# Performance work log

Measured on AMD Instinct MI355X. Metric: run time of the kernel, lower is better.

The kernel has to match this reference:

```python
import jax, jax.numpy as jnp
import numpy as np

B, P = 8, 768
S = 36                 # sample_points (also deformable offset pairs)
C_IN, C_ADJ = 64, 72   # prior_feat_channels -> adjusted channels
D, G = 512, 4          # fc_hidden_dim, num_groups (= attention heads)
N_OFFSETS, N_STRIPS, DEG = 72, 71, 3


def _bilinear(img, x, y):
    """img: [B,H,W,C]; x,y: [B,N] pixel coords. Bilinear sample, zeros outside."""
    H, W = img.shape[1], img.shape[2]
    x0 = jnp.floor(x); y0 = jnp.floor(y)
    x0i = x0.astype(jnp.int32); y0i = y0.astype(jnp.int32)
    wx1 = x - x0; wy1 = y - y0

    def corner(xi, yi, w):
        valid = (xi >= 0) & (xi < W) & (yi >= 0) & (yi < H)
        xc = jnp.clip(xi, 0, W - 1); yc = jnp.clip(yi, 0, H - 1)
        vals = jax.vmap(lambda f, yy, xx: f[yy, xx])(img, yc, xc)  # [B,N,C]
        return vals * (w * valid)[..., None]

    return (corner(x0i, y0i, (1 - wx1) * (1 - wy1))
            + corner(x0i + 1, y0i, wx1 * (1 - wy1))
            + corner(x0i, y0i + 1, (1 - wx1) * wy1)
            + corner(x0i + 1, y0i + 1, wx1 * wy1))


def _resize_ac(img, Ht, Wt):
    """Bilinear resize with align_corners=True. img: [B,H,W,C]."""
    Bsz, H, W, _ = img.shape
    gy, gx = jnp.meshgrid(jnp.linspace(0.0, H - 1.0, Ht),
                          jnp.linspace(0.0, W - 1.0, Wt), indexing='ij')
    xf = jnp.broadcast_to(gx.reshape(-1), (Bsz, Ht * Wt))
    yf = jnp.broadcast_to(gy.reshape(-1), (Bsz, Ht * Wt))
    return _bilinear(img, xf, yf).reshape(Bsz, Ht, Wt, -1)


def setup_inputs():
    ks = jax.random.split(jax.random.key(0), 32)
    r = lambda i, shp, s=1.0: jax.random.normal(ks[i], shp, dtype=jnp.float32) * s
    z = lambda shp: jnp.zeros(shp, jnp.float32)
    return {
        'feat0': r(0, (B, C_IN, 40, 100)),
        'feat1': r(1, (B, C_IN, 20, 50)),
        'feat2': r(2, (B, C_IN, 10, 25)),
        'priors': jax.random.uniform(ks[3], (B, P, 4 + N_OFFSETS), dtype=jnp.float32) * N_STRIPS,
        'ca_w': r(4, (C_ADJ, C_IN), 0.125), 'ca_b': z((C_ADJ,)),
        'off_w': r(5, (2 * S, C_ADJ), 0.01), 'off_b': r(6, (2 * S,), 0.01),
        'dp_w': r(7, (C_ADJ, C_ADJ), 0.167), 'dp_b': z((C_ADJ,)),
        'z_emb': r(8, (S,), 0.3) + 1.0,
        'gf_w': r(9, (D, S // G, C_ADJ), 0.02), 'gf_b': z((D,)),
        'wq': r(10, (D, D), 0.044), 'bq': z((D,)),
        'wk': r(11, (D, D), 0.044), 'bk': z((D,)),
        'wv': r(12, (D, D), 0.044), 'bv': z((D,)),
        'wo': r(13, (D, D), 0.044), 'bo': z((D,)),
        'cf_w1': r(14, (2 * D, D), 0.044), 'cf_b1': z((2 * D,)),
        'cf_w2': r(15, (D, 2 * D), 0.031), 'cf_b2': z((D,)),
        'cls_w1': r(16, (D, D), 0.044), 'cls_b1': z((D,)),
        'cls_w2': r(17, (2, D), 0.001), 'cls_b2': z((2,)),
        'reg_w1': r(18, (D, D), 0.044), 'reg_b1': z((D,)),
        'p_w1': r(19, (2 * D, D), 0.044), 'p_b1': z((2 * D,)),
        'p_w2': r(20, (DEG + 1, 2 * D), 0.031), 'p_b2': z((DEG + 1,)),
        'b_scale': jnp.ones((1,), jnp.float32), 'b_bias': z((1,)),
    }


def reference(feat0, feat1, feat2, priors, ca_w, ca_b, off_w, off_b, dp_w, dp_b,
              z_emb, gf_w, gf_b, wq, bq, wk, bk, wv, bv, wo, bo,
              cf_w1, cf_b1, cf_w2, cf_b2, cls_w1, cls_b1, cls_w2, cls_b2,
              reg_w1, reg_b1, p_w1, p_b1, p_w2, p_b2, b_scale, b_bias):
    f32 = jnp.float32
    lin = lambda x, w, b: x @ w.T + b

    # ---- prior sampling grid (CLRNet-style) ----
    sx_idx = jnp.floor(jnp.linspace(0.0, 1.0, S) * N_STRIPS).astype(jnp.int32)
    pf_ys = jnp.flip(1.0 - sx_idx.astype(f32) / N_STRIPS)            # [S]
    pf_xs = priors[..., 4 + sx_idx][:, :, ::-1]                       # [B,P,S]
    gx = jnp.clip(pf_xs / N_STRIPS, 0.0, 1.0) * 2.0 - 1.0            # [-1,1]
    gy = jnp.broadcast_to(pf_ys * 2.0 - 1.0, gx.shape)

    # ---- channel adjust (1x1 conv) per level, channels-last ----
    adj = lambda f: jnp.einsum('bchw,oc->bhwo', f, ca_w) + ca_b
    feats = [adj(feat0), adj(feat1), adj(feat2)]                      # [B,H,W,C_ADJ]
    offs0 = jnp.einsum('bhwc,oc->bhwo', feats[0], off_w) + off_b     # [B,H0,W0,2S]

    # ---- deformable multi-level sampling: per (prior, point) gather + 1x1 proj ----
    sidx = jnp.arange(S)
    levels = []
    for l, fl in enumerate(feats):
        Hl, Wl = fl.shape[1], fl.shape[2]
        offs = offs0 if l == 0 else _resize_ac(offs0, Hl, Wl)
        px = (gx + 1.0) * 0.5 * (Wl - 1)
        py = (gy + 1.0) * 0.5 * (Hl - 1)
        ov = _bilinear(offs, px.reshape(B, -1), py.reshape(B, -1)).reshape(B, P, S, S, 2)
        dyx = ov[:, :, sidx, sidx, :]                                 # offset pair s for point s
        sxp = (px + dyx[..., 1]).reshape(B, -1)
        syp = (py + dyx[..., 0]).reshape(B, -1)
        smp = _bilinear(fl, sxp, syp).reshape(B, P, S, C_ADJ)
        levels.append(smp @ dp_w.T + dp_b)
    feat_all = jnp.stack(levels)                                      # [3,B,P,S,C]

    # ---- z-embedding soft level selection ----
    zw = jax.nn.softmax(-(z_emb[:, None] - jnp.arange(3, dtype=f32)) ** 2 / 2.0, axis=-1)  # [S,3]
    feature = jnp.einsum('lbpsc,sl->bpsc', feat_all, zw)

    # ---- grouped gather Conv1d(S -> D, kernel=C_ADJ, groups=G) ----
    xg = feature.reshape(B * P, G, S // G, C_ADJ)
    wg = gf_w.reshape(G, D // G, S // G, C_ADJ)
    feature = (jnp.einsum('ngik,goik->ngo', xg, wg).reshape(B * P, D) + gf_b).reshape(B, P, D)

    # ---- multi-head self-attention over priors + channel MLP residual ----
    dh = D // G
    q = lin(feature, wq, bq).reshape(B, P, G, dh).transpose(0, 2, 1, 3)
    k = lin(feature, wk, bk).reshape(B, P, G, dh).transpose(0, 2, 1, 3)
    v = lin(feature, wv, bv).reshape(B, P, G, dh).transpose(0, 2, 1, 3)
    attn = jax.nn.softmax(jnp.einsum('bgqd,bgkd->bgqk', q, k) / float(np.sqrt(dh)), axis=-1)
    res = jnp.einsum('bgqk,bgkd->bgqd', attn, v).transpose(0, 2, 1, 3).reshape(B, P, D)
    res = lin(res, wo, bo)
    feature = feature + lin(jax.nn.relu(lin(res, cf_w1, cf_b1)), cf_w2, cf_b2)

    # ---- heads ----
    fc = feature.reshape(B * P, D)
    cls_logits = lin(jax.nn.relu(lin(fc, cls_w1, cls_b1)), cls_w2, cls_b2).reshape(B, P, 2)
    reg = jax.nn.relu(lin(fc, reg_w1, reg_b1)).reshape(B, P, D)
    coeffs = lin(jax.nn.relu(lin(reg, p_w1, p_b1)), p_w2, p_b2)       # [B,P,DEG+1]
    coeffs = jnp.concatenate([coeffs[..., :2], coeffs[..., 2:] * b_scale + b_bias], axis=-1)
    ys = jnp.linspace(0.0, 1.0, N_OFFSETS)
    basis = jnp.stack([ys ** i for i in range(DEG + 1)], axis=1)      # [N_OFFSETS, DEG+1]
    xs_pred = jax.nn.sigmoid(jnp.einsum('bnd,od->bno', coeffs, basis))
    return jnp.concatenate([cls_logits, coeffs, xs_pred], axis=-1)    # [B,P,78]
```

## Files before the change

### kernel.cpp

```cpp
#include <hip/hip_runtime.h>
#include <hip/hip_bf16.h>
#include <math.h>

#define BB 8
#define PP 768
#define NPRI 76
#define SS 36
#define CIN 64
#define CADJ 72
#define DD 512

#define H0 40
#define W0 100
#define H1 20
#define W1 50
#define H2 10
#define W2 25

typedef __attribute__((ext_vector_type(8))) short bf16x8;
typedef __attribute__((ext_vector_type(4))) short bf16x4;
typedef __attribute__((ext_vector_type(4))) float f32x4;
#define MFMA_BF16 __builtin_amdgcn_mfma_f32_16x16x32_bf16

typedef const __attribute__((address_space(1))) unsigned int* gas_t;
typedef __attribute__((address_space(3))) unsigned int* las_t;

__device__ __forceinline__ __hip_bfloat16 to_bf16(float v) { return __float2bfloat16(v); }
__device__ __forceinline__ float bf2f(__hip_bfloat16 v) { return __bfloat162float(v); }
__device__ __forceinline__ short to_bf16s(float v) {
    __hip_bfloat16 h = __float2bfloat16(v);
    return *reinterpret_cast<short*>(&h);
}

__device__ __forceinline__ float bsample(const float* __restrict__ img, int H, int W,
                                         int C, int c, float x, float y)
{
    float x0f = floorf(x), y0f = floorf(y);
    int x0 = (int)x0f, y0 = (int)y0f;
    float wx1 = x - x0f, wy1 = y - y0f;
    float wx0 = 1.0f - wx1, wy0 = 1.0f - wy1;
    int xc0 = min(max(x0, 0), W - 1);
    int xc1 = min(max(x0 + 1, 0), W - 1);
    int yc0 = min(max(y0, 0), H - 1);
    int yc1 = min(max(y0 + 1, 0), H - 1);
    bool vx0 = (x0 >= 0) && (x0 < W);
    bool vx1 = (x0 + 1 >= 0) && (x0 + 1 < W);
    bool vy0 = (y0 >= 0) && (y0 < H);
    bool vy1 = (y0 + 1 >= 0) && (y0 + 1 < H);
    float w00 = (vx0 && vy0) ? wx0 * wy0 : 0.0f;
    float w01 = (vx1 && vy0) ? wx1 * wy0 : 0.0f;
    float w10 = (vx0 && vy1) ? wx0 * wy1 : 0.0f;
    float w11 = (vx1 && vy1) ? wx1 * wy1 : 0.0f;
    return w00 * img[((size_t)yc0 * W + xc0) * C + c]
         + w01 * img[((size_t)yc0 * W + xc1) * C + c]
         + w10 * img[((size_t)yc1 * W + xc0) * C + c]
         + w11 * img[((size_t)yc1 * W + xc1) * C + c];
}

__global__ __launch_bounds__(256) void k_wprep(
    const float* __restrict__ wq, const float* __restrict__ wk, const float* __restrict__ wv,
    const float* __restrict__ wo, const float* __restrict__ cf_w1, const float* __restrict__ cf_w2,
    const float* __restrict__ cls_w1, const float* __restrict__ reg_w1, const float* __restrict__ p_w1,
    const float* __restrict__ bq, const float* __restrict__ bk, const float* __restrict__ bv,
    const float* __restrict__ cls_b1, const float* __restrict__ reg_b1,
    const float* __restrict__ gf_w, const float* __restrict__ dp_w,
    const float* __restrict__ dp_b, const float* __restrict__ gf_b,
    __hip_bfloat16* __restrict__ wqkv, __hip_bfloat16* __restrict__ wo_bf,
    __hip_bfloat16* __restrict__ cf1_bf, __hip_bfloat16* __restrict__ cf2_bf,
    __hip_bfloat16* __restrict__ clsreg_bf, __hip_bfloat16* __restrict__ p1_bf,
    __hip_bfloat16* __restrict__ gfw2, float* __restrict__ b2,
    float* __restrict__ bqkv, float* __restrict__ bclsreg)
{
    __shared__ float dpS[CADJ][CADJ + 1];
    __shared__ float gfr[648];
    const int bid = blockIdx.x;
    const int tid = threadIdx.x;

    if (bid < 512) {
        const int o = bid;
        for (int i = tid; i < CADJ * CADJ; i += 256) dpS[i / CADJ][i % CADJ] = dp_w[i];
        for (int i = tid; i < 648; i += 256) gfr[i] = gf_w[(size_t)o * 648 + i];
        __syncthreads();
        for (int t = tid; t < 672; t += 256) {
            float acc = 0.0f;
            if (t < 648) {
                const int i = t / 72, m = t % 72;
                const float* gr = gfr + i * 72;
#pragma unroll 8
                for (int k = 0; k < 72; ++k) acc = fmaf(gr[k], dpS[k][m], acc);
            }
            gfw2[(size_t)o * 672 + t] = to_bf16(acc);
        }
        return;
    }
    if (bid < 514) {
        const int o = (bid - 512) * 256 + tid;
        if (o < DD) {
            const float* gr = gf_w + (size_t)o * 648;
            float acc = gf_b[o];
            for (int j = 0; j < 648; ++j) acc = fmaf(gr[j], dp_b[j % 72], acc);
            b2[o] = acc;
        }
        return;
    }
    long i = (long)(bid - 514) * 256 + tid;
    if (i < 262144) { wqkv[i] = to_bf16(wq[i]); return; }
    i -= 262144;
    if (i < 262144) { wqkv[262144 + i] = to_bf16(wk[i]); return; }
    i -= 262144;
    if (i < 262144) { wqkv[524288 + i] = to_bf16(wv[i]); return; }
    i -= 262144;
    if (i < 262144) { wo_bf[i] = to_bf16(wo[i]); return; }
    i -= 262144;
    if (i < 524288) { cf1_bf[i] = to_bf16(cf_w1[i]); return; }
    i -= 524288;
    if (i < 524288) { cf2_bf[i] = to_bf16(cf_w2[i]); return; }
    i -= 524288;
    if (i < 262144) { clsreg_bf[i] = to_bf16(cls_w1[i]); return; }
    i -= 262144;
    if (i < 262144) { clsreg_bf[262144 + i] = to_bf16(reg_w1[i]); return; }
    i -= 262144;
    if (i < 524288) { p1_bf[i] = to_bf16(p_w1[i]); return; }
    i -= 524288;
    if (i < 512) { bqkv[i] = bq[i]; return; }
    if (i < 1024) { bqkv[i] = bk[i - 512]; return; }
    if (i < 1536) { bqkv[i] = bv[i - 1024]; return; }
    i -= 1536;
    if (i < 512) { bclsreg[i] = cls_b1[i]; return; }
    if (i < 1024) { bclsreg[i] = reg_b1[i - 512]; return; }
}

__global__ __launch_bounds__(256) void k_adjoff(
    const float* __restrict__ f, const float* __restrict__ caw, const float* __restrict__ cab,
    const float* __restrict__ offw, const float* __restrict__ offb,
    float* __restrict__ feout, float* __restrict__ offout, int HW, int do_off)
{
    __shared__ float inS[64][65];
    __shared__ float wS[72][64];
    __shared__ float owS[72][73];
    __shared__ float feS[64][73];
    __shared__ float cabS[72], obS[72];

    const int tid = threadIdx.x;
    const int b = blockIdx.y;
    const int pix0 = blockIdx.x * 64;
    const int cnt = min(64, HW - pix0);
    const int px = tid & 63, og = tid >> 6, o0 = og * 18;

    const float* fb = f + (size_t)b * CIN * HW + pix0;
    for (int i = tid; i < 72 * 64; i += 256) wS[i >> 6][i & 63] = caw[i];
    if (do_off)
        for (int i = tid; i < 72 * 72; i += 256) owS[i / 72][i % 72] = offw[i];
    if (tid < 72) { cabS[tid] = cab[tid]; obS[tid] = do_off ? offb[tid] : 0.f; }
    for (int i = tid; i < 64 * 64; i += 256) {
        const int c = i >> 6, p = i & 63;
        inS[c][p] = (p < cnt) ? fb[(size_t)c * HW + p] : 0.f;
    }
    __syncthreads();

    float acc[18];
#pragma unroll
    for (int j = 0; j < 18; ++j) acc[j] = cabS[o0 + j];
#pragma unroll 4
    for (int c = 0; c < 64; ++c) {
        const float v = inS[c][px];
#pragma unroll
        for (int j = 0; j < 18; ++j) acc[j] = fmaf(v, wS[o0 + j][c], acc[j]);
    }
#pragma unroll
    for (int j = 0; j < 18; ++j) feS[px][o0 + j] = acc[j];
    __syncthreads();

    float* feg = feout + ((size_t)b * HW + pix0) * CADJ;
    for (int i = tid; i < cnt * CADJ; i += 256) feg[i] = feS[i / CADJ][i % CADJ];

    if (!do_off) return;

    float acc2[18];
#pragma unroll
    for (int j = 0; j < 18; ++j) acc2[j] = obS[o0 + j];
#pragma unroll 4
    for (int c = 0; c < 72; ++c) {
        const float v = feS[px][c];
#pragma unroll
        for (int j = 0; j < 18; ++j) acc2[j] = fmaf(v, owS[o0 + j][c], acc2[j]);
    }
    __syncthreads();
#pragma unroll
    for (int j = 0; j < 18; ++j) feS[px][o0 + j] = acc2[j];
    __syncthreads();
    float* ofg = offout + ((size_t)b * HW + pix0) * CADJ;
    for (int i = tid; i < cnt * CADJ; i += 256) ofg[i] = feS[i / CADJ][i % CADJ];
}

__global__ __launch_bounds__(256) void k_resize2(const float* __restrict__ src,
    float* __restrict__ of1, float* __restrict__ of2)
{
    const int T1 = BB * H1 * W1 * CADJ;
    const int T2 = BB * H2 * W2 * CADJ;
    int idx = blockIdx.x * 256 + threadIdx.x;
    if (idx < T1) {
        const int c = idx % CADJ;
        const int j = (idx / CADJ) % W1;
        const int i = (idx / (CADJ * W1)) % H1;
        const int b = idx / (CADJ * W1 * H1);
        float sy = fminf((float)i * ((float)(H0 - 1) / (float)(H1 - 1)), (float)(H0 - 1));
        float sx = fminf((float)j * ((float)(W0 - 1) / (float)(W1 - 1)), (float)(W0 - 1));
        of1[idx] = bsample(src + (size_t)b * H0 * W0 * CADJ, H0, W0, CADJ, c, sx, sy);
        return;
    }
    idx -= T1;
    if (idx >= T2) return;
    const int c = idx % CADJ;
    const int j = (idx / CADJ) % W2;
    const int i = (idx / (CADJ * W2)) % H2;
    const int b = idx / (CADJ * W2 * H2);
    float sy = fminf((float)i * ((float)(H0 - 1) / (float)(H2 - 1)), (float)(H0 - 1));
    float sx = fminf((float)j * ((float)(W0 - 1) / (float)(W2 - 1)), (float)(W0 - 1));
    of2[idx] = bsample(src + (size_t)b * H0 * W0 * CADJ, H0, W0, CADJ, c, sx, sy);
}

__global__ __launch_bounds__(256) void k_sample(
    const float* __restrict__ priors,
    const float* __restrict__ feats0, const float* __restrict__ feats1, const float* __restrict__ feats2,
    const float* __restrict__ offs0,  const float* __restrict__ offs1,  const float* __restrict__ offs2,
    const float* __restrict__ z_emb,
    __hip_bfloat16* __restrict__ fsout)
{
    const int bid = blockIdx.x;
    const int gi = (bid & 7) * 384 + (bid >> 3);
    const int bp0 = gi * 2;
    const int b = bp0 / PP;
    const int tid = threadIdx.x;

    __shared__ int   ib[2][3][SS][4];
    __shared__ float wz[2][3][SS][4];

    const int Hs[3] = {H0, H1, H2};
    const int Wsz[3] = {W0, W1, W2};
    const float* Fb[3] = { feats0 + (size_t)b * H0 * W0 * CADJ,
                           feats1 + (size_t)b * H1 * W1 * CADJ,
                           feats2 + (size_t)b * H2 * W2 * CADJ };
    const float* Ob[3] = { offs0 + (size_t)b * H0 * W0 * CADJ,
                           offs1 + (size_t)b * H1 * W1 * CADJ,
                           offs2 + (size_t)b * H2 * W2 * CADJ };

    if (tid < 2 * 3 * SS) {
        const int p = tid / 108;
        const int l = (tid % 108) / SS;
        const int s = tid % SS;
        const int bp = bp0 + p;
        const float t = (float)(35 - s) / 35.0f;
        const int m = (int)floorf(t * 71.0f);
        const float pfx = priors[(size_t)bp * NPRI + 4 + m];
        const float gxv = fminf(fmaxf(pfx / 71.0f, 0.0f), 1.0f) * 2.0f - 1.0f;
        const float gyv = (1.0f - (float)m / 71.0f) * 2.0f - 1.0f;
        const float z = z_emb[s];
        const float e0 = expf(-0.5f * z * z);
        const float e1 = expf(-0.5f * (z - 1.0f) * (z - 1.0f));
        const float e2 = expf(-0.5f * (z - 2.0f) * (z - 2.0f));
        const float inv = 1.0f / (e0 + e1 + e2);
        const float ev[3] = {e0, e1, e2};
        const float zwl = ev[l] * inv;

        const int Hl = Hs[l], Wl = Wsz[l];
        const float px = (gxv + 1.0f) * 0.5f * (float)(Wl - 1);
        const float py = (gyv + 1.0f) * 0.5f * (float)(Hl - 1);
        const float dy = bsample(Ob[l], Hl, Wl, CADJ, 2 * s,     px, py);
        const float dx = bsample(Ob[l], Hl, Wl, CADJ, 2 * s + 1, px, py);
        const float sx = px + dx, sy = py + dy;
        const float x0f = floorf(sx), y0f = floorf(sy);
        const int x0 = (int)x0f, y0 = (int)y0f;
        const float wx1 = sx - x0f, wy1 = sy - y0f;
        const float wx0 = 1.0f - wx1, wy0 = 1.0f - wy1;
        const bool vx0 = (x0 >= 0) && (x0 < Wl);
        const bool vx1 = (x0 + 1 >= 0) && (x0 + 1 < Wl);
        const bool vy0 = (y0 >= 0) && (y0 < Hl);
        const bool vy1 = (y0 + 1 >= 0) && (y0 + 1 < Hl);
        const int xc0 = min(max(x0, 0), Wl - 1);
        const int xc1 = min(max(x0 + 1, 0), Wl - 1);
        const int yc0 = min(max(y0, 0), Hl - 1);
        const int yc1 = min(max(y0 + 1, 0), Hl - 1);
        wz[p][l][s][0] = ((vx0 && vy0) ? wx0 * wy0 : 0.0f) * zwl;
        wz[p][l][s][1] = ((vx1 && vy0) ? wx1 * wy0 : 0.0f) * zwl;
        wz[p][l][s][2] = ((vx0 && vy1) ? wx0 * wy1 : 0.0f) * zwl;
        wz[p][l][s][3] = ((vx1 && vy1) ? wx1 * wy1 : 0.0f) * zwl;
        ib[p][l][s][0] = (yc0 * Wl + xc0) * CADJ;
        ib[p][l][s][1] = (yc0 * Wl + xc1) * CADJ;
        ib[p][l][s][2] = (yc1 * Wl + xc0) * CADJ;
        ib[p][l][s][3] = (yc1 * Wl + xc1) * CADJ;
    }
    __syncthreads();

    for (int idx = tid; idx < 2 * SS * 18; idx += 256) {
        const int p = idx / 648;
        const int rem = idx % 648;
        const int s = rem / 18, k4 = (rem % 18) * 4;
        float a0 = 0.f, a1 = 0.f, a2 = 0.f, a3 = 0.f;
#pragma unroll
        for (int l = 0; l < 3; ++l) {
            const float* F = Fb[l];
            const int*   ibs = ib[p][l][s];
            const float* ws  = wz[p][l][s];
#pragma unroll
            for (int c = 0; c < 4; ++c) {
                const float4 v = *(const float4*)(F + ibs[c] + k4);
                a0 = fmaf(ws[c], v.x, a0);
                a1 = fmaf(ws[c], v.y, a1);
                a2 = fmaf(ws[c], v.z, a2);
                a3 = fmaf(ws[c], v.w, a3);
            }
        }
        bf16x4 pk;
        pk[0] = to_bf16s(a0); pk[1] = to_bf16s(a1);
        pk[2] = to_bf16s(a2); pk[3] = to_bf16s(a3);
        __hip_bfloat16* orow = fsout + (size_t)(bp0 + p) * 2688;
        *(bf16x4*)&orow[(s / 9) * 672 + (s % 9) * 72 + k4] = pk;
    }
    if (tid < 2 * 96) {
        const int p = tid / 96, g = (tid % 96) / 24, t = tid % 24;
        fsout[(size_t)(bp0 + p) * 2688 + g * 672 + 648 + t] = to_bf16(0.0f);
    }
}

__global__ __launch_bounds__(256) void k_bgemm(
    const __hip_bfloat16* __restrict__ A, int lda, long sAz,
    const __hip_bfloat16* __restrict__ W, int ldw, long sWz,
    const float* __restrict__ bias, int sBz,
    const __hip_bfloat16* __restrict__ Res, int ldres,
    __hip_bfloat16* __restrict__ C, int ldc, int sCz,
    int K, int relu)
{
    __shared__ __hip_bfloat16 As[128][32];
    __shared__ __hip_bfloat16 Bs[128][32];
    const int tid = threadIdx.x;
    const int lane = tid & 63, w = tid >> 6;
    const int wr = w >> 1, wc = w & 1;
    const int row16 = lane & 15, kg = lane >> 4;
    const int z = blockIdx.z;
    const int m0 = blockIdx.y * 128, n0 = blockIdx.x * 128;
    const __hip_bfloat16* Ab = A + (size_t)z * sAz;
    const __hip_bfloat16* Wb = W + (size_t)z * sWz;
    const int gr = lane >> 2;
    const int gc = (lane & 3) * 8;

    f32x4 acc[4][4];
#pragma unroll
    for (int i = 0; i < 4; ++i)
#pragma unroll
        for (int j = 0; j < 4; ++j) acc[i][j] = (f32x4){0.f, 0.f, 0.f, 0.f};

    for (int k0 = 0; k0 < K; k0 += 32) {
        __syncthreads();
#pragma unroll
        for (int c = 0; c < 2; ++c) {
            const int r = w * 32 + c * 16;
            __builtin_amdgcn_global_load_lds(
                (gas_t)(Ab + (size_t)(m0 + r + gr) * lda + k0 + gc),
                (las_t)&As[r][0], 16, 0, 0);
            __builtin_amdgcn_global_load_lds(
                (gas_t)(Wb + (size_t)(n0 + r + gr) * ldw + k0 + gc),
                (las_t)&Bs[r][0], 16, 0, 0);
        }
        __syncthreads();
        bf16x8 af[4], bfr[4];
#pragma unroll
        for (int i = 0; i < 4; ++i) af[i]  = *(const bf16x8*)&As[wr * 64 + i * 16 + row16][kg * 8];
#pragma unroll
        for (int j = 0; j < 4; ++j) bfr[j] = *(const bf16x8*)&Bs[wc * 64 + j * 16 + row16][kg * 8];
#pragma unroll
        for (int i = 0; i < 4; ++i)
#pragma unroll
            for (int j = 0; j < 4; ++j)
                acc[i][j] = MFMA_BF16(af[i], bfr[j], acc[i][j], 0, 0, 0);
    }

    const float* bz = bias + (size_t)z * sBz;
    __hip_bfloat16* Cz = C + (size_t)z * sCz;
#pragma unroll
    for (int i = 0; i < 4; ++i) {
#pragma unroll
        for (int r = 0; r < 4; ++r) {
            const int row = m0 + wr * 64 + i * 16 + kg * 4 + r;
#pragma unroll
            for (int j = 0; j < 4; ++j) {
                const int col = n0 + wc * 64 + j * 16 + row16;
                float v = acc[i][j][r] + bz[col];
                if (Res) v += bf2f(Res[(size_t)row * ldres + col]);
                if (relu) v = fmaxf(v, 0.0f);
                Cz[(size_t)row * ldc + col] = to_bf16(v);
            }
        }
    }
}

__global__ __launch_bounds__(256) void k_bgemm64(
    const __hip_bfloat16* __restrict__ A, int lda, long sAz,
    const __hip_bfloat16* __restrict__ W, int ldw, long sWz,
    const float* __restrict__ bias, int sBz,
    const __hip_bfloat16* __restrict__ Res, int ldres,
    __hip_bfloat16* __restrict__ C, int ldc, int sCz,
    int K, int relu)
{
    __shared__ __hip_bfloat16 As[2][64][32];
    __shared__ __hip_bfloat16 Bs[2][64][32];
    const int tid = threadIdx.x;
    const int lane = tid & 63, w = tid >> 6;
    const int wr = w >> 1, wc = w & 1;
    const int row16 = lane & 15, kg = lane >> 4;
    const int z = blockIdx.z;
    const int m0 = blockIdx.y * 64, n0 = blockIdx.x * 64;
    const __hip_bfloat16* Ab = A + (size_t)z * sAz;
    const __hip_bfloat16* Wb = W + (size_t)z * sWz;
    const int gr = lane >> 2;
    const int gc = (lane & 3) * 8;

    f32x4 acc[2][2];
#pragma unroll
    for (int i = 0; i < 2; ++i)
#pragma unroll
        for (int j = 0; j < 2; ++j) acc[i][j] = (f32x4){0.f, 0.f, 0.f, 0.f};

    __builtin_amdgcn_global_load_lds(
        (gas_t)(Ab + (size_t)(m0 + w * 16 + gr) * lda + gc),
        (las_t)&As[0][w * 16][0], 16, 0, 0);
    __builtin_amdgcn_global_load_lds(
        (gas_t)(Wb + (size_t)(n0 + w * 16 + gr) * ldw + gc),
        (las_t)&Bs[0][w * 16][0], 16, 0, 0);
    __syncthreads();

    int cur = 0;
    for (int k0 = 0; k0 < K; k0 += 32) {
        if (k0 + 32 < K) {
            const int nxt = cur ^ 1;
            __builtin_amdgcn_global_load_lds(
                (gas_t)(Ab + (size_t)(m0 + w * 16 + gr) * lda + k0 + 32 + gc),
                (las_t)&As[nxt][w * 16][0], 16, 0, 0);
            __builtin_amdgcn_global_load_lds(
                (gas_t)(Wb + (size_t)(n0 + w * 16 + gr) * ldw + k0 + 32 + gc),
                (las_t)&Bs[nxt][w * 16][0], 16, 0, 0);
        }
        bf16x8 af[2], bfr[2];
#pragma unroll
        for (int i = 0; i < 2; ++i) af[i]  = *(const bf16x8*)&As[cur][wr * 32 + i * 16 + row16][kg * 8];
#pragma unroll
        for (int j = 0; j < 2; ++j) bfr[j] = *(const bf16x8*)&Bs[cur][wc * 32 + j * 16 + row16][kg * 8];
#pragma unroll
        for (int i = 0; i < 2; ++i)
#pragma unroll
            for (int j = 0; j < 2; ++j)
                acc[i][j] = MFMA_BF16(af[i], bfr[j], acc[i][j], 0, 0, 0);
        __syncthreads();
        cur ^= 1;
    }

    const float* bz = bias + (size_t)z * sBz;
    __hip_bfloat16* Cz = C + (size_t)z * sCz;
#pragma unroll
    for (int i = 0; i < 2; ++i) {
#pragma unroll
        for (int r = 0; r < 4; ++r) {
            const int row = m0 + wr * 32 + i * 16 + kg * 4 + r;
#pragma unroll
            for (int j = 0; j < 2; ++j) {
                const int col = n0 + wc * 32 + j * 16 + row16;
                float v = acc[i][j][r] + bz[col];
                if (Res) v += bf2f(Res[(size_t)row * ldres + col]);
                if (relu) v = fmaxf(v, 0.0f);
                Cz[(size_t)row * ldc + col] = to_bf16(v);
            }
        }
    }
}

__global__ __launch_bounds__(256) void k_vt(
    const __hip_bfloat16* __restrict__ qkv, __hip_bfloat16* __restrict__ Vt)
{
    const int kt = blockIdx.x;
    const int bg = blockIdx.y;
    const int b = bg >> 2, g = bg & 3;
    const int tid = threadIdx.x;
    __shared__ unsigned short Vs[64][130];

    const __hip_bfloat16* src = qkv + (size_t)(b * PP + kt * 64) * 1536 + 1024 + g * 128;
    for (int i = tid; i < 1024; i += 256) {
        const int row = i >> 4, ch = i & 15;
        *(bf16x8*)&Vs[row][ch * 8] = *(const bf16x8*)(src + (size_t)row * 1536 + ch * 8);
    }
    __syncthreads();
    __hip_bfloat16* dst = Vt + (size_t)bg * 128 * 768 + kt * 64;
    for (int i = tid; i < 1024; i += 256) {
        const int d = i >> 3, kc = i & 7;
        bf16x8 pk;
#pragma unroll
        for (int j = 0; j < 8; ++j) pk[j] = (short)Vs[kc * 8 + j][d];
        *(bf16x8*)(dst + (size_t)d * 768 + kc * 8) = pk;
    }
}

__global__ __launch_bounds__(256) void k_fattn(
    const __hip_bfloat16* __restrict__ qkv, const __hip_bfloat16* __restrict__ Vt,
    __hip_bfloat16* __restrict__ Out)
{
    const int id = blockIdx.x;
    const int xcd = id & 7, rest = id >> 3;
    const int bg = xcd * 4 + rest / 12;
    const int qt = rest % 12;
    const int b = bg >> 2, g = bg & 3;
    const int tid = threadIdx.x, lane = tid & 63, w = tid >> 6;
    const int row16 = lane & 15, kg = lane >> 4;
    const int q0 = qt * 64;

    __shared__ __hip_bfloat16 Klds[64][136];
    __shared__ __hip_bfloat16 Vtl[128][72];
    __shared__ __hip_bfloat16 Plds[4][16][72];

    const size_t rowQ = (size_t)(b * PP + q0 + w * 16 + row16) * 1536 + g * 128;
    bf16x8 aq[4];
#pragma unroll
    for (int t = 0; t < 4; ++t)
        aq[t] = *(const bf16x8*)(qkv + rowQ + t * 32 + kg * 8);

    f32x4 oacc[8];
#pragma unroll
    for (int dt = 0; dt < 8; ++dt) oacc[dt] = (f32x4){0.f, 0.f, 0.f, 0.f};
    float mrow[4] = {-3.0e38f, -3.0e38f, -3.0e38f, -3.0e38f};
    float lrow[4] = {0.f, 0.f, 0.f, 0.f};

    const __hip_bfloat16* Kb = qkv + (size_t)(b * PP) * 1536 + 512 + g * 128;
    const __hip_bfloat16* Vb = Vt + (size_t)bg * 128 * 768;
    const float sc = 0.08838834764831845f;

    const int krow = tid >> 2, kch = tid & 3;
    const int vrow = tid >> 1, vch = tid & 1;
    bf16x8 kreg[4], vreg[4];

    {
        const __hip_bfloat16* s1 = Kb + (size_t)krow * 1536 + kch * 32;
        const __hip_bfloat16* s2 = Vb + (size_t)vrow * 768 + vch * 32;
#pragma unroll
        for (int j = 0; j < 4; ++j) { kreg[j] = *(const bf16x8*)(s1 + j * 8);
                                      vreg[j] = *(const bf16x8*)(s2 + j * 8); }
    }

    for (int kt = 0; kt < 12; ++kt) {
        __syncthreads();
#pragma unroll
        for (int j = 0; j < 4; ++j) {
            *(bf16x8*)&Klds[krow][kch * 32 + j * 8] = kreg[j];
            *(bf16x8*)&Vtl[vrow][vch * 32 + j * 8] = vreg[j];
        }
        __syncthreads();
        if (kt < 11) {
            const __hip_bfloat16* s1 = Kb + (size_t)((kt + 1) * 64 + krow) * 1536 + kch * 32;
            const __hip_bfloat16* s2 = Vb + (size_t)vrow * 768 + (kt + 1) * 64 + vch * 32;
#pragma unroll
            for (int j = 0; j < 4; ++j) { kreg[j] = *(const bf16x8*)(s1 + j * 8);
                                          vreg[j] = *(const bf16x8*)(s2 + j * 8); }
        }

        f32x4 s4[4];
#pragma unroll
        for (int st = 0; st < 4; ++st) s4[st] = (f32x4){0.f, 0.f, 0.f, 0.f};
        __builtin_amdgcn_s_setprio(1);
#pragma unroll
        for (int st = 0; st < 4; ++st)
#pragma unroll
            for (int t = 0; t < 4; ++t)
                s4[st] = MFMA_BF16(aq[t],
                    *(const bf16x8*)&Klds[st * 16 + row16][t * 32 + kg * 8], s4[st], 0, 0, 0);
        __builtin_amdgcn_s_setprio(0);

        float pm[4];
#pragma unroll
        for (int r = 0; r < 4; ++r) {
            float m0 = fmaxf(fmaxf(s4[0][r], s4[1][r]), fmaxf(s4[2][r], s4[3][r])) * sc;
            m0 = fmaxf(m0, __shfl_xor(m0, 1));
            m0 = fmaxf(m0, __shfl_xor(m0, 2));
            m0 = fmaxf(m0, __shfl_xor(m0, 4));
            m0 = fmaxf(m0, __shfl_xor(m0, 8));
            pm[r] = m0;
        }
        const float need = fmaxf(fmaxf(pm[0] - mrow[0], pm[1] - mrow[1]),
                                 fmaxf(pm[2] - mrow[2], pm[3] - mrow[3]));
        if (!__all(need <= 8.0f)) {
#pragma unroll
            for (int r = 0; r < 4; ++r) {
                const float mn = fmaxf(mrow[r], pm[r]);
                const float so = __expf(mrow[r] - mn);
                lrow[r] *= so;
#pragma unroll
                for (int dt = 0; dt < 8; ++dt) oacc[dt][r] *= so;
                mrow[r] = mn;
            }
        }
#pragma unroll
        for (int r = 0; r < 4; ++r) {
            float rs = 0.f;
#pragma unroll
            for (int st = 0; st < 4; ++st) {
                const float p = __expf(s4[st][r] * sc - mrow[r]);
                rs += p;
                Plds[w][kg * 4 + r][st * 16 + row16] = to_bf16(p);
            }
            rs += __shfl_xor(rs, 1);
            rs += __shfl_xor(rs, 2);
            rs += __shfl_xor(rs, 4);
            rs += __shfl_xor(rs, 8);
            lrow[r] += rs;
        }

        __builtin_amdgcn_s_setprio(1);
#pragma unroll
        for (int ks = 0; ks < 2; ++ks) {
            bf16x8 ap = *(const bf16x8*)&Plds[w][row16][ks * 32 + kg * 8];
#pragma unroll
            for (int dt = 0; dt < 8; ++dt)
                oacc[dt] = MFMA_BF16(ap,
                    *(const bf16x8*)&Vtl[dt * 16 + row16][ks * 32 + kg * 8], oacc[dt], 0, 0, 0);
        }
        __builtin_amdgcn_s_setprio(0);
    }

    const size_t obase = (size_t)(b * PP + q0 + w * 16 + kg * 4) * DD + g * 128;
#pragma unroll
    for (int r = 0; r < 4; ++r) {
        const float inv = 1.0f / lrow[r];
#pragma unroll
        for (int dt = 0; dt < 8; ++dt)
            Out[obase + (size_t)r * DD + dt * 16 + row16] = to_bf16(oacc[dt][r] * inv);
    }
}

__global__ __launch_bounds__(64) void k_head(
    const __hip_bfloat16* __restrict__ clsreg, const __hip_bfloat16* __restrict__ ph,
    const float* __restrict__ cls_w2, const float* __restrict__ cls_b2,
    const float* __restrict__ p_w2, const float* __restrict__ p_b2,
    const float* __restrict__ b_scale, const float* __restrict__ b_bias,
    float* __restrict__ outp)
{
    const int bp = blockIdx.x;
    const int lane = threadIdx.x;
    const __hip_bfloat16* hr = clsreg + (size_t)bp * 1024;
    float a0 = 0.0f, a1 = 0.0f;
    for (int i = lane; i < DD; i += 64) {
        float h = bf2f(hr[i]);
        a0 = fmaf(h, cls_w2[i], a0);
        a1 = fmaf(h, cls_w2[DD + i], a1);
    }
    const __hip_bfloat16* pr = ph + (size_t)bp * 1024;
    float c0 = 0.0f, c1 = 0.0f, c2 = 0.0f, c3 = 0.0f;
    for (int i = lane; i < 1024; i += 64) {
        float h = bf2f(pr[i]);
        c0 = fmaf(h, p_w2[i], c0);
        c1 = fmaf(h, p_w2[1024 + i], c1);
        c2 = fmaf(h, p_w2[2048 + i], c2);
        c3 = fmaf(h, p_w2[3072 + i], c3);
    }
#pragma unroll
    for (int off = 32; off > 0; off >>= 1) {
        a0 += __shfl_down(a0, off);
        a1 += __shfl_down(a1, off);
        c0 += __shfl_down(c0, off);
        c1 += __shfl_down(c1, off);
        c2 += __shfl_down(c2, off);
        c3 += __shfl_down(c3, off);
    }
    a0 = __shfl(a0, 0); a1 = __shfl(a1, 0);
    c0 = __shfl(c0, 0); c1 = __shfl(c1, 0);
    c2 = __shfl(c2, 0); c3 = __shfl(c3, 0);
    const float k0 = c0 + p_b2[0];
    const float k1 = c1 + p_b2[1];
    const float scv = b_scale[0], biv = b_bias[0];
    const float k2 = (c2 + p_b2[2]) * scv + biv;
    const float k3 = (c3 + p_b2[3]) * scv + biv;
    float* orow = outp + (size_t)bp * 78;
    if (lane == 0) {
        orow[0] = a0 + cls_b2[0];
        orow[1] = a1 + cls_b2[1];
        orow[2] = k0; orow[3] = k1; orow[4] = k2; orow[5] = k3;
    }
    for (int o = lane; o < 72; o += 64) {
        float ys = (float)o / 71.0f;
        float tv = k0 + ys * (k1 + ys * (k2 + ys * k3));
        orow[6 + o] = 1.0f / (1.0f + expf(-tv));
    }
}

extern "C" void kernel_launch(void* const* d_in, const int* in_sizes, int n_in,
                              void* d_out, int out_size, void* d_ws, size_t ws_size,
                              hipStream_t stream)
{
    const float* feat0  = (const float*)d_in[0];
    const float* feat1  = (const float*)d_in[1];
    const float* feat2  = (const float*)d_in[2];
    const float* priors = (const float*)d_in[3];
    const float* ca_w   = (const float*)d_in[4];
    const float* ca_b   = (const float*)d_in[5];
    const float* off_w  = (const float*)d_in[6];
    const float* off_b  = (const float*)d_in[7];
    const float* dp_w   = (const float*)d_in[8];
    const float* dp_b   = (const float*)d_in[9];
    const float* z_emb  = (const float*)d_in[10];
    const float* gf_w   = (const float*)d_in[11];
    const float* gf_b   = (const float*)d_in[12];
    const float* wq     = (const float*)d_in[13];
    const float* bq     = (const float*)d_in[14];
    const float* wk     = (const float*)d_in[15];
    const float* bk     = (const float*)d_in[16];
    const float* wv     = (const float*)d_in[17];
    const float* bv     = (const float*)d_in[18];
    const float* wo     = (const float*)d_in[19];
    const float* bo     = (const float*)d_in[20];
    const float* cf_w1  = (const float*)d_in[21];
    const float* cf_b1  = (const float*)d_in[22];
    const float* cf_w2  = (const float*)d_in[23];
    const float* cf_b2  = (const float*)d_in[24];
    const float* cls_w1 = (const float*)d_in[25];
    const float* cls_b1 = (const float*)d_in[26];
    const float* cls_w2 = (const float*)d_in[27];
    const float* cls_b2 = (const float*)d_in[28];
    const float* reg_w1 = (const float*)d_in[29];
    const float* reg_b1 = (const float*)d_in[30];
    const float* p_w1   = (const float*)d_in[31];
    const float* p_b1   = (const float*)d_in[32];
    const float* p_w2   = (const float*)d_in[33];
    const float* p_b2   = (const float*)d_in[34];
    const float* b_scale = (const float*)d_in[35];
    const float* b_bias  = (const float*)d_in[36];
    float* out = (float*)d_out;

    char* wsb = (char*)d_ws;
    __hip_bfloat16* feature = (__hip_bfloat16*)(wsb + 0);
    __hip_bfloat16* qkvb    = (__hip_bfloat16*)(wsb + 6291456);
    __hip_bfloat16* tb      = (__hip_bfloat16*)(wsb + 25165824);
    __hip_bfloat16* vtb     = (__hip_bfloat16*)(wsb + 31457280);
    __hip_bfloat16* rb      = (__hip_bfloat16*)(wsb + 31457280);
    __hip_bfloat16* hb      = (__hip_bfloat16*)(wsb + 37748736);
    __hip_bfloat16* f2      = (__hip_bfloat16*)(wsb + 50331648);
    __hip_bfloat16* clsregb = (__hip_bfloat16*)(wsb + 56623104);
    __hip_bfloat16* phb     = (__hip_bfloat16*)(wsb + 69206016);
    float* of1 = (float*)(wsb + 6291456);
    float* of2 = (float*)(wsb + 8595456);
    float* fe1 = (float*)(wsb + 9171456);
    float* fe2 = (float*)(wsb + 11475456);
    __hip_bfloat16* fsb = (__hip_bfloat16*)(wsb + 25165824);
    float* fe0 = (float*)(wsb + 58195968);
    float* of0 = (float*)(wsb + 67411968);
    __hip_bfloat16* wqkv_bf   = (__hip_bfloat16*)(wsb + 81788928);
    __hip_bfloat16* wo_bf     = (__hip_bfloat16*)(wsb + 83361792);
    __hip_bfloat16* cf1_bf    = (__hip_bfloat16*)(wsb + 83886080);
    __hip_bfloat16* cf2_bf    = (__hip_bfloat16*)(wsb + 84934656);
    __hip_bfloat16* clsreg_bf = (__hip_bfloat16*)(wsb + 85983232);
    __hip_bfloat16* p1_bf     = (__hip_bfloat16*)(wsb + 87031808);
    __hip_bfloat16* gfw2_bf   = (__hip_bfloat16*)(wsb + 88080384);
    float* bqkv    = (float*)(wsb + 88768512);
    float* bclsreg = (float*)(wsb + 88774656);
    float* b2      = (float*)(wsb + 88778752);

    k_wprep<<<12812, 256, 0, stream>>>(
        wq, wk, wv, wo, cf_w1, cf_w2, cls_w1, reg_w1, p_w1, bq, bk, bv, cls_b1, reg_b1,
        gf_w, dp_w, dp_b, gf_b,
        wqkv_bf, wo_bf, cf1_bf, cf2_bf, clsreg_bf, p1_bf, gfw2_bf, b2, bqkv, bclsreg);

    k_adjoff<<<dim3(63, BB), 256, 0, stream>>>(feat0, ca_w, ca_b, off_w, off_b,
                                               fe0, of0, H0 * W0, 1);
    k_adjoff<<<dim3(16, BB), 256, 0, stream>>>(feat1, ca_w, ca_b, off_w, off_b,
                                               fe1, nullptr, H1 * W1, 0);
    k_adjoff<<<dim3(4, BB), 256, 0, stream>>>(feat2, ca_w, ca_b, off_w, off_b,
                                              fe2, nullptr, H2 * W2, 0);
    k_resize2<<<(BB * (H1 * W1 + H2 * W2) * CADJ + 255) / 256, 256, 0, stream>>>(of0, of1, of2);
    k_sample<<<3072, 256, 0, stream>>>(priors, fe0, fe1, fe2, of0, of1, of2, z_emb, fsb);

    const int M = BB * PP;
    k_bgemm64<<<dim3(2, M / 64, 4), 256, 0, stream>>>(
        fsb, 2688, 672, gfw2_bf, 672, 128 * 672, b2, 128,
        nullptr, 0, feature, DD, 128, 672, 0);
    k_bgemm<<<dim3(12, M / 128, 1), 256, 0, stream>>>(
        feature, DD, 0, wqkv_bf, DD, 0, bqkv, 0,
        nullptr, 0, qkvb, 1536, 0, DD, 0);
    k_vt<<<dim3(12, 32), 256, 0, stream>>>(qkvb, vtb);
    k_fattn<<<384, 256, 0, stream>>>(qkvb, vtb, tb);
    k_bgemm64<<<dim3(8, M / 64, 1), 256, 0, stream>>>(
        tb, DD, 0, wo_bf, DD, 0, bo, 0, nullptr, 0, rb, DD, 0, DD, 0);
    k_bgemm64<<<dim3(16, M / 64, 1), 256, 0, stream>>>(
        rb, DD, 0, cf1_bf, DD, 0, cf_b1, 0, nullptr, 0, hb, 1024, 0, DD, 1);
    k_bgemm64<<<dim3(8, M / 64, 1), 256, 0, stream>>>(
        hb, 1024, 0, cf2_bf, 1024, 0, cf_b2, 0, feature, DD, f2, DD, 0, 1024, 0);
    k_bgemm64<<<dim3(16, M / 64, 1), 256, 0, stream>>>(
        f2, DD, 0, clsreg_bf, DD, 0, bclsreg, 0, nullptr, 0, clsregb, 1024, 0, DD, 1);
    k_bgemm64<<<dim3(16, M / 64, 1), 256, 0, stream>>>(
        clsregb + 512, 1024, 0, p1_bf, DD, 0, p_b1, 0, nullptr, 0, phb, 1024, 0, DD, 1);

    k_head<<<M, 64, 0, stream>>>(clsregb, phb, cls_w2, cls_b2, p_w2, p_b2, b_scale, b_bias, out);
}
```

Before: 306.4 us.

## Deepen bgemm64 K-tile to 64 and pad grouped GEMM K to 704

```diff
diff --git a/kernel.cpp b/kernel.cpp
--- a/kernel.cpp
+++ b/kernel.cpp
@@ -16,6 +16,9 @@
 #define W1 50
 #define H2 10
 #define W2 25
+
+#define GK 704
+#define FSLD 2816
 
 typedef __attribute__((ext_vector_type(8))) short bf16x8;
 typedef __attribute__((ext_vector_type(4))) short bf16x4;
@@ -81,7 +84,7 @@
         for (int i = tid; i < CADJ * CADJ; i += 256) dpS[i / CADJ][i % CADJ] = dp_w[i];
         for (int i = tid; i < 648; i += 256) gfr[i] = gf_w[(size_t)o * 648 + i];
         __syncthreads();
-        for (int t = tid; t < 672; t += 256) {
+        for (int t = tid; t < GK; t += 256) {
             float acc = 0.0f;
             if (t < 648) {
                 const int i = t / 72, m = t % 72;
@@ -89,7 +92,7 @@
 #pragma unroll 8
                 for (int k = 0; k < 72; ++k) acc = fmaf(gr[k], dpS[k][m], acc);
             }
-            gfw2[(size_t)o * 672 + t] = to_bf16(acc);
+            gfw2[(size_t)o * GK + t] = to_bf16(acc);
         }
         return;
     }
@@ -296,30 +299,34 @@
         const int p = idx / 648;
         const int rem = idx % 648;
         const int s = rem / 18, k4 = (rem % 18) * 4;
+        float4 vv[12];
+        float  wv[12];
+#pragma unroll
+        for (int l = 0; l < 3; ++l)
+#pragma unroll
+            for (int c = 0; c < 4; ++c) {
+                vv[l * 4 + c] = *(const float4*)(Fb[l] + ib[p][l][s][c] + k4);
+                wv[l * 4 + c] = wz[p][l][s][c];
+            }
         float a0 = 0.f, a1 = 0.f, a2 = 0.f, a3 = 0.f;
 #pragma unroll
-        for (int l = 0; l < 3; ++l) {
-            const float* F = Fb[l];
-            const int*   ibs = ib[p][l][s];
-            const float* ws  = wz[p][l][s];
-#pragma unroll
-            for (int c = 0; c < 4; ++c) {
-                const float4 v = *(const float4*)(F + ibs[c] + k4);
-                a0 = fmaf(ws[c], v.x, a0);
-                a1 = fmaf(ws[c], v.y, a1);
-                a2 = fmaf(ws[c], v.z, a2);
-                a3 = fmaf(ws[c], v.w, a3);
-            }
+        for (int t = 0; t < 12; ++t) {
+            a0 = fmaf(wv[t], vv[t].x, a0);
+            a1 = fmaf(wv[t], vv[t].y, a1);
+            a2 = fmaf(wv[t], vv[t].z, a2);
+            a3 = fmaf(wv[t], vv[t].w, a3);
         }
         bf16x4 pk;
         pk[0] = to_bf16s(a0); pk[1] = to_bf16s(a1);
         pk[2] = to_bf16s(a2); pk[3] = to_bf16s(a3);
-        __hip_bfloat16* orow = fsout + (size_t)(bp0 + p) * 2688;
-        *(bf16x4*)&orow[(s / 9) * 672 + (s % 9) * 72 + k4] = pk;
-    }
-    if (tid < 2 * 96) {
-        const int p = tid / 96, g = (tid % 96) / 24, t = tid % 24;
-        fsout[(size_t)(bp0 + p) * 2688 + g * 672 + 648 + t] = to_bf16(0.0f);
+        __hip_bfloat16* orow = fsout + (size_t)(bp0 + p) * FSLD;
+        *(bf16x4*)&orow[(s / 9) * GK + (s % 9) * 72 + k4] = pk;
+    }
+    for (int t2 = tid; t2 < 2 * 4 * (GK - 648); t2 += 256) {
+        const int p = t2 / (4 * (GK - 648));
+        const int r = t2 % (4 * (GK - 648));
+        const int g = r / (GK - 648), t = r % (GK - 648);
+        fsout[(size_t)(bp0 + p) * FSLD + g * GK + 648 + t] = to_bf16(0.0f);
     }
 }
 
@@ -402,8 +409,8 @@
     __hip_bfloat16* __restrict__ C, int ldc, int sCz,
     int K, int relu)
 {
-    __shared__ __hip_bfloat16 As[2][64][32];
-    __shared__ __hip_bfloat16 Bs[2][64][32];
+    __shared__ __hip_bfloat16 As[2][64][64];
+    __shared__ __hip_bfloat16 Bs[2][64][64];
     const int tid = threadIdx.x;
     const int lane = tid & 63, w = tid >> 6;
     const int wr = w >> 1, wc = w & 1;
@@ -412,8 +419,22 @@
     const int m0 = blockIdx.y * 64, n0 = blockIdx.x * 64;
     const __hip_bfloat16* Ab = A + (size_t)z * sAz;
     const __hip_bfloat16* Wb = W + (size_t)z * sWz;
-    const int gr = lane >> 2;
-    const int gc = (lane & 3) * 8;
+    const int grow = lane >> 3;
+    const int gc = (lane & 7) * 8;
+
+#define STAGE64(buf, kbase)                                                        \
+    {                                                                              \
+        _Pragma("unroll")                                                          \
+        for (int inst = 0; inst < 2; ++inst) {                                     \
+            const int rb = inst * 32 + w * 8;                                      \
+            __builtin_amdgcn_global_load_lds(                                      \
+                (gas_t)(Ab + (size_t)(m0 + rb + grow) * lda + (kbase) + gc),       \
+                (las_t)&As[buf][rb][0], 16, 0, 0);                                 \
+            __builtin_amdgcn_global_load_lds(                                      \
+                (gas_t)(Wb + (size_t)(n0 + rb + grow) * ldw + (kbase) + gc),       \
+                (las_t)&Bs[buf][rb][0], 16, 0, 0);                                 \
+        }                                                                          \
+    }
 
     f32x4 acc[2][2];
 #pragma unroll
@@ -421,38 +442,31 @@
 #pragma unroll
         for (int j = 0; j < 2; ++j) acc[i][j] = (f32x4){0.f, 0.f, 0.f, 0.f};
 
-    __builtin_amdgcn_global_load_lds(
-        (gas_t)(Ab + (size_t)(m0 + w * 16 + gr) * lda + gc),
-        (las_t)&As[0][w * 16][0], 16, 0, 0);
-    __builtin_amdgcn_global_load_lds(
-        (gas_t)(Wb + (size_t)(n0 + w * 16 + gr) * ldw + gc),
-        (las_t)&Bs[0][w * 16][0], 16, 0, 0);
+    STAGE64(0, 0)
     __syncthreads();
 
     int cur = 0;
-    for (int k0 = 0; k0 < K; k0 += 32) {
-        if (k0 + 32 < K) {
-            const int nxt = cur ^ 1;
-            __builtin_amdgcn_global_load_lds(
-                (gas_t)(Ab + (size_t)(m0 + w * 16 + gr) * lda + k0 + 32 + gc),
-                (las_t)&As[nxt][w * 16][0], 16, 0, 0);
-            __builtin_amdgcn_global_load_lds(
-                (gas_t)(Wb + (size_t)(n0 + w * 16 + gr) * ldw + k0 + 32 + gc),
-                (las_t)&Bs[nxt][w * 16][0], 16, 0, 0);
-        }
-        bf16x8 af[2], bfr[2];
-#pragma unroll
-        for (int i = 0; i < 2; ++i) af[i]  = *(const bf16x8*)&As[cur][wr * 32 + i * 16 + row16][kg * 8];
-#pragma unroll
-        for (int j = 0; j < 2; ++j) bfr[j] = *(const bf16x8*)&Bs[cur][wc * 32 + j * 16 + row16][kg * 8];
+    for (int k0 = 0; k0 < K; k0 += 64) {
+        if (k0 + 64 < K) STAGE64(cur ^ 1, k0 + 64)
+        bf16x8 af[2][2], bfr[2][2];
 #pragma unroll
         for (int i = 0; i < 2; ++i)
 #pragma unroll
-            for (int j = 0; j < 2; ++j)
-                acc[i][j] = MFMA_BF16(af[i], bfr[j], acc[i][j], 0, 0, 0);
+            for (int kk = 0; kk < 2; ++kk) {
+                af[i][kk]  = *(const bf16x8*)&As[cur][wr * 32 + i * 16 + row16][kk * 32 + kg * 8];
+                bfr[i][kk] = *(const bf16x8*)&Bs[cur][wc * 32 + i * 16 + row16][kk * 32 + kg * 8];
+            }
+#pragma unroll
+        for (int kk = 0; kk < 2; ++kk)
+#pragma unroll
+            for (int i = 0; i < 2; ++i)
+#pragma unroll
+                for (int j = 0; j < 2; ++j)
+                    acc[i][j] = MFMA_BF16(af[i][kk], bfr[j][kk], acc[i][j], 0, 0, 0);
         __syncthreads();
         cur ^= 1;
     }
+#undef STAGE64
 
     const float* bz = bias + (size_t)z * sBz;
     __hip_bfloat16* Cz = C + (size_t)z * sCz;
@@ -745,8 +759,8 @@
     float* fe1 = (float*)(wsb + 9171456);
     float* fe2 = (float*)(wsb + 11475456);
     __hip_bfloat16* fsb = (__hip_bfloat16*)(wsb + 25165824);
-    float* fe0 = (float*)(wsb + 58195968);
-    float* of0 = (float*)(wsb + 67411968);
+    float* fe0 = (float*)(wsb + 59768832);
+    float* of0 = (float*)(wsb + 68984832);
     __hip_bfloat16* wqkv_bf   = (__hip_bfloat16*)(wsb + 81788928);
     __hip_bfloat16* wo_bf     = (__hip_bfloat16*)(wsb + 83361792);
     __hip_bfloat16* cf1_bf    = (__hip_bfloat16*)(wsb + 83886080);
@@ -754,9 +768,9 @@
     __hip_bfloat16* clsreg_bf = (__hip_bfloat16*)(wsb + 85983232);
     __hip_bfloat16* p1_bf     = (__hip_bfloat16*)(wsb + 87031808);
     __hip_bfloat16* gfw2_bf   = (__hip_bfloat16*)(wsb + 88080384);
-    float* bqkv    = (float*)(wsb + 88768512);
-    float* bclsreg = (float*)(wsb + 88774656);
-    float* b2      = (float*)(wsb + 88778752);
+    float* bqkv    = (float*)(wsb + 88801280);
+    float* bclsreg = (float*)(wsb + 88807424);
+    float* b2      = (float*)(wsb + 88811520);
 
     k_wprep<<<12812, 256, 0, stream>>>(
         wq, wk, wv, wo, cf_w1, cf_w2, cls_w1, reg_w1, p_w1, bq, bk, bv, cls_b1, reg_b1,
@@ -774,8 +788,8 @@
 
     const int M = BB * PP;
     k_bgemm64<<<dim3(2, M / 64, 4), 256, 0, stream>>>(
-        fsb, 2688, 672, gfw2_bf, 672, 128 * 672, b2, 128,
-        nullptr, 0, feature, DD, 128, 672, 0);
+        fsb, FSLD, GK, gfw2_bf, GK, 128 * GK, b2, 128,
+        nullptr, 0, feature, DD, 128, GK, 0);
     k_bgemm<<<dim3(12, M / 128, 1), 256, 0, stream>>>(
         feature, DD, 0, wqkv_bf, DD, 0, bqkv, 0,
         nullptr, 0, qkvb, 1536, 0, DD, 0);
```

Result: slower. 320.0 us (+4.4%).
